# Kernel tuning notes

Measured on AMD Instinct MI355X. Metric: run time of the kernel, lower is better.

Reference implementation:

```python
import jax, jax.numpy as jnp
import numpy as np

B, T, C = 4, 2048, 2048
H, HKV = 16, 4
D = C // H            # 128
G = H // HKV          # 4 query heads per kv head
ROPE_THETA = 10000.0


def _rope_tables(seq_len, head_dim, theta):
    inv = 1.0 / (theta ** (np.arange(0, head_dim, 2, dtype=np.float32) / head_dim))
    t = np.arange(seq_len, dtype=np.float32)
    f = np.outer(t, inv)  # (T, D/2)
    return jnp.asarray(np.cos(f)), jnp.asarray(np.sin(f))


def setup_inputs() -> dict:
    key = jax.random.key(0)
    ks = jax.random.split(key, 5)
    x = jax.random.normal(ks[0], (B, T, C), dtype=jnp.float32)
    W_q = jax.random.normal(ks[1], (H * D, C), dtype=jnp.float32) * 0.02
    W_k = jax.random.normal(ks[2], (HKV * D, C), dtype=jnp.float32) * 0.02
    W_v = jax.random.normal(ks[3], (HKV * D, C), dtype=jnp.float32) * 0.02
    W_o = jax.random.normal(ks[4], (C, C), dtype=jnp.float32) * 0.02
    cos, sin = _rope_tables(T, D, ROPE_THETA)
    return {"x": x, "W_q": W_q, "W_k": W_k, "W_v": W_v, "W_o": W_o,
            "cos": cos, "sin": sin}


def _apply_rope(xh, cos, sin):
    # xh: (B, h, T, D); cos/sin: (T, D/2)
    x0 = xh[..., 0::2]
    x1 = xh[..., 1::2]
    c = cos[None, None, :, :]
    s = sin[None, None, :, :]
    o0 = x0 * c - x1 * s
    o1 = x0 * s + x1 * c
    return jnp.stack([o0, o1], axis=-1).reshape(xh.shape)


def reference(x, W_q, W_k, W_v, W_o, cos, sin):
    b, t, c = x.shape
    q = (x @ W_q.T).reshape(b, t, H, D).transpose(0, 2, 1, 3)      # (B,H,T,D)
    k = (x @ W_k.T).reshape(b, t, HKV, D).transpose(0, 2, 1, 3)    # (B,HKV,T,D)
    v = (x @ W_v.T).reshape(b, t, HKV, D).transpose(0, 2, 1, 3)
    q = _apply_rope(q, cos[:t], sin[:t])
    k = _apply_rope(k, cos[:t], sin[:t])
    # GQA via reshape instead of repeat_interleave (same head ordering:
    # q head index h = kv*G + g).
    qg = q.reshape(b, HKV, G, t, D)
    scores = jnp.einsum('bkgtd,bksd->bkgts', qg, k) / jnp.sqrt(jnp.float32(D))
    causal = jnp.tril(jnp.ones((t, t), dtype=bool))
    scores = jnp.where(causal[None, None, None, :, :], scores, -jnp.inf)
    attn = jax.nn.softmax(scores, axis=-1)
    out = jnp.einsum('bkgts,bksd->bkgtd', attn, v)                 # (B,HKV,G,T,D)
    out = out.reshape(b, H, t, D).transpose(0, 2, 1, 3).reshape(b, t, c)
    return out @ W_o.T
```

## Files before the change

kernel.cpp:

```cpp
#include <hip/hip_runtime.h>
#include <cmath>

typedef __attribute__((ext_vector_type(8))) short bf16x8;
typedef __attribute__((ext_vector_type(4))) float f32x4;
typedef __attribute__((ext_vector_type(16))) float f32x16;
typedef unsigned short u16;

__device__ __forceinline__ u16 f2bf(float f) {
  union { float f; unsigned u; } x; x.f = f;
  return (u16)((x.u + 0x7FFFu + ((x.u >> 16) & 1u)) >> 16);
}

__device__ __forceinline__ unsigned cvtpk(float lo, float hi) {
  unsigned r;
  asm("v_cvt_pk_bf16_f32 %0, %1, %2" : "=v"(r) : "v"(lo), "v"(hi));
  return r;
}

__device__ __forceinline__ void gload_lds16(const void* g, void* l) {
  __builtin_amdgcn_global_load_lds((const __attribute__((address_space(1))) unsigned*)g,
                                   (__attribute__((address_space(3))) unsigned*)l,
                                   16, 0, 0);
}

__global__ __launch_bounds__(256) void cast_all_kernel(const float* __restrict__ x,
                                                       const float* __restrict__ wq,
                                                       const float* __restrict__ wk,
                                                       const float* __restrict__ wv,
                                                       const float* __restrict__ wo,
                                                       u16* __restrict__ out) {
  const long b1 = 16777216, b2 = 20971520, b3 = 22020096, b4 = 23068672, b5 = 27262976;
  long i = (long)blockIdx.x * blockDim.x + threadIdx.x;
  long stride = (long)gridDim.x * blockDim.x;
  for (long j = i * 4; j < b5; j += stride * 4) {
    const float* src; long off;
    if (j < b1)      { src = x;  off = j; }
    else if (j < b2) { src = wq; off = j - b1; }
    else if (j < b3) { src = wk; off = j - b2; }
    else if (j < b4) { src = wv; off = j - b3; }
    else             { src = wo; off = j - b4; }
    float4 v = *(const float4*)(src + off);
    ushort4 o;
    o.x = f2bf(v.x); o.y = f2bf(v.y); o.z = f2bf(v.z); o.w = f2bf(v.w);
    *(ushort4*)(out + j) = o;
  }
}

template <int EPI>
__global__ __launch_bounds__(512, 2) void gemm_bt256(const u16* __restrict__ A,
                                                     const u16* __restrict__ B,
                                                     void* __restrict__ outp,
                                                     int M, int N, int K,
                                                     const float* __restrict__ cosp,
                                                     const float* __restrict__ sinp,
                                                     float scale) {
  __shared__ u16 lds[65536];
  const int tid = threadIdx.x;
  const int lane = tid & 63;
  const int l16 = lane & 15, lhi = lane >> 4;
  const int w = tid >> 6;
  const int wr = w >> 2, wc = w & 3;
  const int m0 = blockIdx.y * 256;
  const int n0 = blockIdx.x * 256;

  f32x4 acc[8][4];
#pragma unroll
  for (int i = 0; i < 8; ++i)
#pragma unroll
    for (int j = 0; j < 4; ++j) acc[i][j] = (f32x4)0.0f;

  const int NT = K >> 6;

  auto stage = [&](int t, int buf) {
    const int k0 = t << 6;
    u16* Ad = lds + buf * 32768;
    u16* Bd = Ad + 16384;
#pragma unroll
    for (int j = 0; j < 4; ++j) {
      int c = tid + j * 512;
      int row = c >> 3;
      int sboff = ((c & 7) * 16) ^ ((row & 7) << 4);
      gload_lds16(A + (size_t)(m0 + row) * K + k0 + (sboff >> 1), Ad + (size_t)c * 8);
    }
#pragma unroll
    for (int j = 0; j < 4; ++j) {
      int c = tid + j * 512;
      int row = c >> 3;
      int sboff = ((c & 7) * 16) ^ ((row & 7) << 4);
      gload_lds16(B + (size_t)(n0 + row) * K + k0 + (sboff >> 1), Bd + (size_t)c * 8);
    }
  };

  stage(0, 0);
  stage(1, 1);

  for (int t = 0; t < NT; ++t) {
    const int cur = t & 1;
    if (t + 1 < NT) { asm volatile("s_waitcnt vmcnt(8)" ::: "memory"); }
    else            { asm volatile("s_waitcnt vmcnt(0)" ::: "memory"); }
    __builtin_amdgcn_s_barrier();
    const char* Ab = (const char*)(lds + cur * 32768);
    const char* Bb = (const char*)(lds + cur * 32768 + 16384);
#pragma unroll
    for (int qm = 0; qm < 2; ++qm)
#pragma unroll
      for (int qn = 0; qn < 2; ++qn) {
        bf16x8 af[4][2], bfr[2][2];
#pragma unroll
        for (int mi = 0; mi < 4; ++mi) {
          int ra = wr * 128 + qm * 64 + mi * 16 + l16;
#pragma unroll
          for (int kk = 0; kk < 2; ++kk)
            af[mi][kk] = *(const bf16x8*)(Ab + ra * 128 + ((kk * 64 + lhi * 16) ^ ((ra & 7) << 4)));
        }
#pragma unroll
        for (int ni = 0; ni < 2; ++ni) {
          int rb = wc * 64 + qn * 32 + ni * 16 + l16;
#pragma unroll
          for (int kk = 0; kk < 2; ++kk)
            bfr[ni][kk] = *(const bf16x8*)(Bb + rb * 128 + ((kk * 64 + lhi * 16) ^ ((rb & 7) << 4)));
        }
        __builtin_amdgcn_s_setprio(1);
#pragma unroll
        for (int kk = 0; kk < 2; ++kk)
#pragma unroll
          for (int mi = 0; mi < 4; ++mi)
#pragma unroll
            for (int ni = 0; ni < 2; ++ni)
              acc[qm * 4 + mi][qn * 2 + ni] = __builtin_amdgcn_mfma_f32_16x16x32_bf16(
                  af[mi][kk], bfr[ni][kk], acc[qm * 4 + mi][qn * 2 + ni], 0, 0, 0);
        __builtin_amdgcn_s_setprio(0);
      }
    asm volatile("s_waitcnt lgkmcnt(0)" ::: "memory");
    __builtin_amdgcn_s_barrier();
    if (t + 2 < NT) stage(t + 2, cur);
  }

  if (EPI == 2) {
    float* o = (float*)outp;
#pragma unroll
    for (int mi8 = 0; mi8 < 8; ++mi8)
#pragma unroll
      for (int r = 0; r < 4; ++r) {
        int row = m0 + wr * 128 + mi8 * 16 + lhi * 4 + r;
#pragma unroll
        for (int nj = 0; nj < 4; ++nj) {
          int col = n0 + wc * 64 + nj * 16 + l16;
          o[(size_t)row * N + col] = acc[mi8][nj][r];
        }
      }
  } else {
    u16* o = (u16*)outp;
    const int nheads = N >> 7;
#pragma unroll
    for (int mi8 = 0; mi8 < 8; ++mi8)
#pragma unroll
      for (int r = 0; r < 4; ++r) {
        int row = m0 + wr * 128 + mi8 * 16 + lhi * 4 + r;
        int b = row >> 11;
        int tt = row & 2047;
#pragma unroll
        for (int nj = 0; nj < 4; ++nj) {
          int col = n0 + wc * 64 + nj * 16 + l16;
          int hh = col >> 7, dd = col & 127;
          float v = acc[mi8][nj][r];
          float p = __shfl_xor(v, 1);
          float c = cosp[tt * 64 + (dd >> 1)];
          float s = sinp[tt * 64 + (dd >> 1)];
          v = (lane & 1) ? fmaf(p, s, v * c) : fmaf(v, c, -p * s);
          v *= scale;
          o[((size_t)(b * nheads + hh) * 2048 + tt) * 128 + dd] = f2bf(v);
        }
      }
  }
}

template <int EPI>
__global__ __launch_bounds__(256) void gemm_bt(const u16* __restrict__ A,
                                               const u16* __restrict__ B,
                                               void* __restrict__ outp,
                                               u16* __restrict__ vtp,
                                               int M, int N, int K,
                                               const float* __restrict__ cosp,
                                               const float* __restrict__ sinp,
                                               float scale) {
  __shared__ u16 As[128 * 64];
  __shared__ u16 Bs[128 * 64];
  const int tid = threadIdx.x;
  const int lane = tid & 63;
  const int l16 = lane & 15, lhi = lane >> 4;
  const int w = tid >> 6;
  const int wr = w >> 1, wc = w & 1;
  const int m0 = blockIdx.y * 128;
  const int n0 = blockIdx.x * 128;
  const int wbase = tid - lane;

  f32x4 acc[4][4];
#pragma unroll
  for (int i = 0; i < 4; ++i)
#pragma unroll
    for (int j = 0; j < 4; ++j) acc[i][j] = (f32x4)0.0f;

  for (int k0 = 0; k0 < K; k0 += 64) {
    __syncthreads();
#pragma unroll
    for (int j = 0; j < 4; ++j) {
      int c = tid + j * 256;
      gload_lds16(A + (size_t)(m0 + (c >> 3)) * K + k0 + (c & 7) * 8,
                  As + (size_t)(wbase + j * 256) * 8);
    }
#pragma unroll
    for (int j = 0; j < 4; ++j) {
      int c = tid + j * 256;
      gload_lds16(B + (size_t)(n0 + (c >> 3)) * K + k0 + (c & 7) * 8,
                  Bs + (size_t)(wbase + j * 256) * 8);
    }
    __syncthreads();
#pragma unroll
    for (int kk = 0; kk < 64; kk += 32) {
      bf16x8 af[4], bfr[4];
#pragma unroll
      for (int mi = 0; mi < 4; ++mi)
        af[mi] = *(const bf16x8*)&As[(wr * 64 + mi * 16 + l16) * 64 + kk + lhi * 8];
#pragma unroll
      for (int ni = 0; ni < 4; ++ni)
        bfr[ni] = *(const bf16x8*)&Bs[(wc * 64 + ni * 16 + l16) * 64 + kk + lhi * 8];
#pragma unroll
      for (int mi = 0; mi < 4; ++mi)
#pragma unroll
        for (int ni = 0; ni < 4; ++ni)
          acc[mi][ni] = __builtin_amdgcn_mfma_f32_16x16x32_bf16(af[mi], bfr[ni], acc[mi][ni], 0, 0, 0);
    }
  }

  {
    const int bx = blockIdx.x;
    if (bx < 4) {
      u16* o = (u16*)outp;
#pragma unroll
      for (int mi = 0; mi < 4; ++mi)
#pragma unroll
        for (int r = 0; r < 4; ++r) {
          int row = m0 + wr * 64 + mi * 16 + lhi * 4 + r;
          int b = row >> 11;
          int t = row & 2047;
          size_t base = ((size_t)(b * 4 + bx) * 2048 + t) * 128;
#pragma unroll
          for (int ni = 0; ni < 4; ++ni) {
            int d = wc * 64 + ni * 16 + l16;
            float v = acc[mi][ni][r];
            float p = __shfl_xor(v, 1);
            float c = cosp[t * 64 + (d >> 1)];
            float s = sinp[t * 64 + (d >> 1)];
            v = (lane & 1) ? fmaf(p, s, v * c) : fmaf(v, c, -p * s);
            o[base + d] = f2bf(v);
          }
        }
    } else {
      const int kvh = bx - 4;
#pragma unroll
      for (int mi = 0; mi < 4; ++mi)
#pragma unroll
        for (int r = 0; r < 4; ++r) {
          int row = m0 + wr * 64 + mi * 16 + lhi * 4 + r;
          int b = row >> 11;
          int t = row & 2047;
          size_t base = ((size_t)(b * 4 + kvh) * 128) * 2048 + t;
#pragma unroll
          for (int ni = 0; ni < 4; ++ni) {
            int d = wc * 64 + ni * 16 + l16;
            vtp[base + (size_t)d * 2048] = f2bf(acc[mi][ni][r]);
          }
        }
    }
  }
}

__global__ __launch_bounds__(512, 2) void attn_kernel(const u16* __restrict__ Q,
                                                      const u16* __restrict__ Kp,
                                                      const u16* __restrict__ Vtp,
                                                      u16* __restrict__ O) {
  __shared__ u16 lds[65536];

  const int tid = threadIdx.x;
  const int lane = tid & 63;
  const int w = tid >> 6;
  const int l5 = lane & 31, hi = lane >> 5;
  const int bid = blockIdx.x;
  const int hb = bid & 63;
  const int pa = bid >> 6;
  const int h = hb >> 2;
  const int b = hb & 3;
  const int kvh = h >> 2;
  const int wbase = tid - lane;

  const u16* Kb = Kp + (size_t)(b * 4 + kvh) * 2048 * 128;
  const u16* Vtb = Vtp + (size_t)(b * 4 + kvh) * 128 * 2048;

  auto stageKV = [&](int kt, int buf) {
    const int t0k = kt * 128;
    u16* Kd = lds + buf * 32768;
    u16* Vd = Kd + 16384;
#pragma unroll
    for (int j = 0; j < 4; ++j) {
      int c = tid + j * 512;
      int row = c >> 4;
      int sboff = ((c & 15) * 16) ^ ((row & 15) << 4);
      gload_lds16(Kb + (size_t)(t0k + row) * 128 + (sboff >> 1),
                  Kd + (size_t)(wbase + j * 512) * 8);
    }
#pragma unroll
    for (int j = 0; j < 4; ++j) {
      int c = tid + j * 512;
      int d = c >> 4;
      int sboff = ((c & 15) * 16) ^ ((d & 7) << 4);
      gload_lds16(Vtb + (size_t)d * 2048 + t0k + (sboff >> 1),
                  Vd + (size_t)(wbase + j * 512) * 8);
    }
  };

  for (int pass = 0; pass < 2; ++pass) {
    const int qt = pass ? (7 - pa) : pa;
    const int q0 = qt * 256;
    const int wrow0 = q0 + w * 32;
    const int qg = wrow0 + l5;

    const u16* Qb = Q + ((size_t)((b * 16 + h) * 2048 + wrow0)) * 128;
    bf16x8 qf[8];
#pragma unroll
    for (int ks = 0; ks < 8; ++ks)
      qf[ks] = *(const bf16x8*)(Qb + (size_t)l5 * 128 + ks * 16 + hi * 8);

    f32x16 oacc[4];
#pragma unroll
    for (int i = 0; i < 4; ++i) oacc[i] = (f32x16)0.0f;
    float m = -3.0e38f, l = 0.0f;

    const int nkt = 2 * qt + 2;
    stageKV(0, 0);

    for (int kt = 0; kt < nkt; ++kt) {
      const int cur = kt & 1;
      if (kt + 1 < nkt) {
        stageKV(kt + 1, cur ^ 1);
        asm volatile("s_waitcnt vmcnt(8)" ::: "memory");
      } else {
        asm volatile("s_waitcnt vmcnt(0)" ::: "memory");
      }
      __builtin_amdgcn_s_barrier();

#pragma unroll
      for (int sub = 0; sub < 2; ++sub) {
        const int t0s = kt * 128 + sub * 64;
        if (t0s <= wrow0 + 31) {
          const char* ksb = (const char*)(lds + cur * 32768 + sub * 8192);
          const char* vtb = (const char*)(lds + cur * 32768 + 16384);
          const int vsub = sub * 128;

          float p[32];
#pragma unroll
          for (int kt2 = 0; kt2 < 2; ++kt2) {
            f32x16 sacc = (f32x16)0.0f;
            int row = kt2 * 32 + l5;
            __builtin_amdgcn_s_setprio(1);
#pragma unroll
            for (int ks = 0; ks < 8; ++ks) {
              bf16x8 kf = *(const bf16x8*)(ksb + row * 256 + ((ks * 32 + hi * 16) ^ ((row & 15) << 4)));
              sacc = __builtin_amdgcn_mfma_f32_32x32x16_bf16(kf, qf[ks], sacc, 0, 0, 0);
            }
            __builtin_amdgcn_s_setprio(0);
#pragma unroll
            for (int r = 0; r < 16; ++r) p[kt2 * 16 + r] = sacc[r];
          }

          if (t0s + 63 > wrow0) {
#pragma unroll
            for (int kt2 = 0; kt2 < 2; ++kt2)
#pragma unroll
              for (int r = 0; r < 16; ++r) {
                int kvg = t0s + kt2 * 32 + (r & 3) + 8 * (r >> 2) + 4 * hi;
                if (kvg > qg) p[kt2 * 16 + r] = -3.0e38f;
              }
          }

          float mx[16];
#pragma unroll
          for (int i = 0; i < 16; ++i) mx[i] = fmaxf(p[i], p[i + 16]);
#pragma unroll
          for (int i = 0; i < 8; ++i) mx[i] = fmaxf(mx[i], mx[i + 8]);
#pragma unroll
          for (int i = 0; i < 4; ++i) mx[i] = fmaxf(mx[i], mx[i + 4]);
          float rm = fmaxf(fmaxf(mx[0], mx[1]), fmaxf(mx[2], mx[3]));
          rm = fmaxf(rm, __shfl_xor(rm, 32));

          bool defer = __all(rm <= m + 8.0f);
          if (!defer) {
            float mnew = fmaxf(m, rm);
            float sc = exp2f(m - mnew);
            m = mnew;
            l *= sc;
#pragma unroll
            for (int i = 0; i < 4; ++i)
#pragma unroll
              for (int r = 0; r < 16; ++r) oacc[i][r] *= sc;
          }

#pragma unroll
          for (int i = 0; i < 32; ++i) p[i] = exp2f(p[i] - m);
          float sm[16];
#pragma unroll
          for (int i = 0; i < 16; ++i) sm[i] = p[i] + p[i + 16];
#pragma unroll
          for (int i = 0; i < 8; ++i) sm[i] += sm[i + 8];
#pragma unroll
          for (int i = 0; i < 4; ++i) sm[i] += sm[i + 4];
          float s2 = (sm[0] + sm[1]) + (sm[2] + sm[3]);
          s2 += __shfl_xor(s2, 32);
          l += s2;

#pragma unroll
          for (int kt2 = 0; kt2 < 2; ++kt2) {
#pragma unroll
            for (int sl = 0; sl < 2; ++sl) {
              int base = kt2 * 16 + sl * 8;
              unsigned A0 = cvtpk(p[base + 0], p[base + 1]);
              unsigned A1 = cvtpk(p[base + 2], p[base + 3]);
              unsigned A2 = cvtpk(p[base + 4], p[base + 5]);
              unsigned A3 = cvtpk(p[base + 6], p[base + 7]);
              asm volatile("v_permlane32_swap_b32 %0, %1" : "+v"(A0), "+v"(A2));
              asm volatile("v_permlane32_swap_b32 %0, %1" : "+v"(A1), "+v"(A3));
              union { unsigned u[4]; bf16x8 v; } pf;
              pf.u[0] = A0;
              pf.u[1] = A1;
              pf.u[2] = A2;
              pf.u[3] = A3;
              int s = kt2 * 2 + sl;
              __builtin_amdgcn_s_setprio(1);
#pragma unroll
              for (int dt = 0; dt < 4; ++dt) {
                int row = dt * 32 + l5;
                bf16x8 vb = *(const bf16x8*)(vtb + row * 256 + vsub +
                                             ((s * 32 + hi * 16) ^ ((row & 7) << 4)));
                oacc[dt] = __builtin_amdgcn_mfma_f32_32x32x16_bf16(vb, pf.v, oacc[dt], 0, 0, 0);
              }
              __builtin_amdgcn_s_setprio(0);
            }
          }
        }
      }

      asm volatile("s_waitcnt lgkmcnt(0)" ::: "memory");
      __builtin_amdgcn_s_barrier();
    }

    float inv = 1.0f / l;
    __syncthreads();
    for (int half = 0; half < 2; ++half) {
      if ((w >> 2) == half) {
        u16* OSw = lds + (w & 3) * 4352;
#pragma unroll
        for (int dt = 0; dt < 4; ++dt)
#pragma unroll
          for (int r = 0; r < 16; ++r) {
            int d = dt * 32 + (r & 3) + 8 * (r >> 2) + 4 * hi;
            OSw[l5 * 136 + d] = f2bf(oacc[dt][r] * inv);
          }
      }
      __syncthreads();
      u16* Ob = O + ((size_t)(b * 2048 + q0 + half * 128)) * 2048 + h * 128;
#pragma unroll
      for (int j = 0; j < 4; ++j) {
        int c = tid + j * 512;
        int row = c >> 4, col = c & 15;
        *(bf16x8*)(Ob + (size_t)row * 2048 + col * 8) =
            *(const bf16x8*)&lds[(row >> 5) * 4352 + (row & 31) * 136 + col * 8];
      }
      __syncthreads();
    }
  }
}

extern "C" void kernel_launch(void* const* d_in, const int* in_sizes, int n_in,
                              void* d_out, int out_size, void* d_ws, size_t ws_size,
                              hipStream_t stream) {
  (void)in_sizes; (void)n_in; (void)out_size; (void)ws_size;
  const float* x    = (const float*)d_in[0];
  const float* Wq   = (const float*)d_in[1];
  const float* Wk   = (const float*)d_in[2];
  const float* Wv   = (const float*)d_in[3];
  const float* Wo   = (const float*)d_in[4];
  const float* cosp = (const float*)d_in[5];
  const float* sinp = (const float*)d_in[6];

  u16* ws  = (u16*)d_ws;
  u16* xbf = ws;
  u16* Wqb = xbf + 16777216;
  u16* Wkb = Wqb + 4194304;
  u16* Wvb = Wkb + 1048576;
  u16* Wob = Wvb + 1048576;
  u16* Qb  = Wob + 4194304;
  u16* Kb  = Qb + 16777216;
  u16* Vb  = Kb + 4194304;
  u16* AO  = xbf;

  cast_all_kernel<<<2048, 256, 0, stream>>>(x, Wq, Wk, Wv, Wo, ws);

  const float qscale = (float)(1.4426950408889634 / sqrt(128.0));

  gemm_bt256<0><<<dim3(8, 32), 512, 0, stream>>>(xbf, Wqb, Qb, 8192, 2048, 2048, cosp, sinp, qscale);
  gemm_bt<3><<<dim3(8, 64), 256, 0, stream>>>(xbf, Wkb, Kb, Vb, 8192, 1024, 2048, cosp, sinp, 1.0f);

  attn_kernel<<<256, 512, 0, stream>>>(Qb, Kb, Vb, AO);

  gemm_bt256<2><<<dim3(8, 32), 512, 0, stream>>>(AO, Wob, d_out, 8192, 2048, 2048, nullptr, nullptr, 1.0f);
}
```

Measured before the change: 317.9 us.

## Double-buffer KV projection GEMM and widen attention softmax block to 128 keys

The K/V projection GEMM now uses two LDS buffers, issuing async global-to-LDS loads two tiles ahead with vmcnt waits in place of a full sync per step. It also raises MFMA priority and sets launch bounds for two blocks per CU. In attention, the online-softmax max, rescale and sum now run once per 128-key tile instead of once per 64-key subtile, halving the reduction and rescale overhead. The cost is more registers for the larger score array and coarser causal skipping, since a 64-key half that is fully masked is no longer skipped on its own.

```diff
diff --git a/kernel.cpp b/kernel.cpp
--- a/kernel.cpp
+++ b/kernel.cpp
@@ -175,17 +175,14 @@
   }
 }
 
-template <int EPI>
-__global__ __launch_bounds__(256) void gemm_bt(const u16* __restrict__ A,
-                                               const u16* __restrict__ B,
-                                               void* __restrict__ outp,
-                                               u16* __restrict__ vtp,
-                                               int M, int N, int K,
-                                               const float* __restrict__ cosp,
-                                               const float* __restrict__ sinp,
-                                               float scale) {
-  __shared__ u16 As[128 * 64];
-  __shared__ u16 Bs[128 * 64];
+__global__ __launch_bounds__(256, 2) void gemm_kv(const u16* __restrict__ A,
+                                                  const u16* __restrict__ B,
+                                                  u16* __restrict__ kp,
+                                                  u16* __restrict__ vtp,
+                                                  int M, int N, int K,
+                                                  const float* __restrict__ cosp,
+                                                  const float* __restrict__ sinp) {
+  __shared__ u16 lds[32768];
   const int tid = threadIdx.x;
   const int lane = tid & 63;
   const int l16 = lane & 15, lhi = lane >> 4;
@@ -201,21 +198,36 @@
 #pragma unroll
     for (int j = 0; j < 4; ++j) acc[i][j] = (f32x4)0.0f;
 
-  for (int k0 = 0; k0 < K; k0 += 64) {
-    __syncthreads();
+  const int NT = K >> 6;
+
+  auto stage = [&](int t, int buf) {
+    const int k0 = t << 6;
+    u16* Ad = lds + buf * 16384;
+    u16* Bd = Ad + 8192;
 #pragma unroll
     for (int j = 0; j < 4; ++j) {
       int c = tid + j * 256;
       gload_lds16(A + (size_t)(m0 + (c >> 3)) * K + k0 + (c & 7) * 8,
-                  As + (size_t)(wbase + j * 256) * 8);
+                  Ad + (size_t)(wbase + j * 256) * 8);
     }
 #pragma unroll
     for (int j = 0; j < 4; ++j) {
       int c = tid + j * 256;
       gload_lds16(B + (size_t)(n0 + (c >> 3)) * K + k0 + (c & 7) * 8,
-                  Bs + (size_t)(wbase + j * 256) * 8);
-    }
-    __syncthreads();
+                  Bd + (size_t)(wbase + j * 256) * 8);
+    }
+  };
+
+  stage(0, 0);
+  stage(1, 1);
+
+  for (int t = 0; t < NT; ++t) {
+    const int cur = t & 1;
+    if (t + 1 < NT) { asm volatile("s_waitcnt vmcnt(8)" ::: "memory"); }
+    else            { asm volatile("s_waitcnt vmcnt(0)" ::: "memory"); }
+    __builtin_amdgcn_s_barrier();
+    const u16* As = lds + cur * 16384;
+    const u16* Bs = As + 8192;
 #pragma unroll
     for (int kk = 0; kk < 64; kk += 32) {
       bf16x8 af[4], bfr[4];
@@ -225,18 +237,22 @@
 #pragma unroll
       for (int ni = 0; ni < 4; ++ni)
         bfr[ni] = *(const bf16x8*)&Bs[(wc * 64 + ni * 16 + l16) * 64 + kk + lhi * 8];
+      __builtin_amdgcn_s_setprio(1);
 #pragma unroll
       for (int mi = 0; mi < 4; ++mi)
 #pragma unroll
         for (int ni = 0; ni < 4; ++ni)
           acc[mi][ni] = __builtin_amdgcn_mfma_f32_16x16x32_bf16(af[mi], bfr[ni], acc[mi][ni], 0, 0, 0);
-    }
+      __builtin_amdgcn_s_setprio(0);
+    }
+    asm volatile("s_waitcnt lgkmcnt(0)" ::: "memory");
+    __builtin_amdgcn_s_barrier();
+    if (t + 2 < NT) stage(t + 2, cur);
   }
 
   {
     const int bx = blockIdx.x;
     if (bx < 4) {
-      u16* o = (u16*)outp;
 #pragma unroll
       for (int mi = 0; mi < 4; ++mi)
 #pragma unroll
@@ -253,7 +269,7 @@
             float c = cosp[t * 64 + (d >> 1)];
             float s = sinp[t * 64 + (d >> 1)];
             v = (lane & 1) ? fmaf(p, s, v * c) : fmaf(v, c, -p * s);
-            o[base + d] = f2bf(v);
+            kp[base + d] = f2bf(v);
           }
         }
     } else {
@@ -340,6 +356,7 @@
     stageKV(0, 0);
 
     for (int kt = 0; kt < nkt; ++kt) {
+      const int t0 = kt * 128;
       const int cur = kt & 1;
       if (kt + 1 < nkt) {
         stageKV(kt + 1, cur ^ 1);
@@ -349,15 +366,13 @@
       }
       __builtin_amdgcn_s_barrier();
 
-#pragma unroll
-      for (int sub = 0; sub < 2; ++sub) {
-        const int t0s = kt * 128 + sub * 64;
-        if (t0s <= wrow0 + 31) {
+      if (t0 <= wrow0 + 31) {
+        const char* vtb = (const char*)(lds + cur * 32768 + 16384);
+
+        float p[2][32];
+#pragma unroll
+        for (int sub = 0; sub < 2; ++sub) {
           const char* ksb = (const char*)(lds + cur * 32768 + sub * 8192);
-          const char* vtb = (const char*)(lds + cur * 32768 + 16384);
-          const int vsub = sub * 128;
-
-          float p[32];
 #pragma unroll
           for (int kt2 = 0; kt2 < 2; ++kt2) {
             f32x16 sacc = (f32x16)0.0f;
@@ -370,63 +385,73 @@
             }
             __builtin_amdgcn_s_setprio(0);
 #pragma unroll
-            for (int r = 0; r < 16; ++r) p[kt2 * 16 + r] = sacc[r];
+            for (int r = 0; r < 16; ++r) p[sub][kt2 * 16 + r] = sacc[r];
           }
-
-          if (t0s + 63 > wrow0) {
+        }
+
+        if (t0 + 127 > wrow0) {
+#pragma unroll
+          for (int sub = 0; sub < 2; ++sub)
 #pragma unroll
             for (int kt2 = 0; kt2 < 2; ++kt2)
 #pragma unroll
               for (int r = 0; r < 16; ++r) {
-                int kvg = t0s + kt2 * 32 + (r & 3) + 8 * (r >> 2) + 4 * hi;
-                if (kvg > qg) p[kt2 * 16 + r] = -3.0e38f;
+                int kvg = t0 + sub * 64 + kt2 * 32 + (r & 3) + 8 * (r >> 2) + 4 * hi;
+                if (kvg > qg) p[sub][kt2 * 16 + r] = -3.0e38f;
               }
-          }
-
-          float mx[16];
-#pragma unroll
-          for (int i = 0; i < 16; ++i) mx[i] = fmaxf(p[i], p[i + 16]);
-#pragma unroll
-          for (int i = 0; i < 8; ++i) mx[i] = fmaxf(mx[i], mx[i + 8]);
-#pragma unroll
-          for (int i = 0; i < 4; ++i) mx[i] = fmaxf(mx[i], mx[i + 4]);
-          float rm = fmaxf(fmaxf(mx[0], mx[1]), fmaxf(mx[2], mx[3]));
-          rm = fmaxf(rm, __shfl_xor(rm, 32));
-
-          bool defer = __all(rm <= m + 8.0f);
-          if (!defer) {
-            float mnew = fmaxf(m, rm);
-            float sc = exp2f(m - mnew);
-            m = mnew;
-            l *= sc;
-#pragma unroll
-            for (int i = 0; i < 4; ++i)
-#pragma unroll
-              for (int r = 0; r < 16; ++r) oacc[i][r] *= sc;
-          }
-
-#pragma unroll
-          for (int i = 0; i < 32; ++i) p[i] = exp2f(p[i] - m);
-          float sm[16];
-#pragma unroll
-          for (int i = 0; i < 16; ++i) sm[i] = p[i] + p[i + 16];
-#pragma unroll
-          for (int i = 0; i < 8; ++i) sm[i] += sm[i + 8];
-#pragma unroll
-          for (int i = 0; i < 4; ++i) sm[i] += sm[i + 4];
-          float s2 = (sm[0] + sm[1]) + (sm[2] + sm[3]);
-          s2 += __shfl_xor(s2, 32);
-          l += s2;
-
+        }
+
+        float mx[16];
+#pragma unroll
+        for (int i = 0; i < 16; ++i)
+          mx[i] = fmaxf(fmaxf(p[0][i], p[0][i + 16]), fmaxf(p[1][i], p[1][i + 16]));
+#pragma unroll
+        for (int i = 0; i < 8; ++i) mx[i] = fmaxf(mx[i], mx[i + 8]);
+#pragma unroll
+        for (int i = 0; i < 4; ++i) mx[i] = fmaxf(mx[i], mx[i + 4]);
+        float rm = fmaxf(fmaxf(mx[0], mx[1]), fmaxf(mx[2], mx[3]));
+        rm = fmaxf(rm, __shfl_xor(rm, 32));
+
+        bool defer = __all(rm <= m + 8.0f);
+        if (!defer) {
+          float mnew = fmaxf(m, rm);
+          float sc = exp2f(m - mnew);
+          m = mnew;
+          l *= sc;
+#pragma unroll
+          for (int i = 0; i < 4; ++i)
+#pragma unroll
+            for (int r = 0; r < 16; ++r) oacc[i][r] *= sc;
+        }
+
+#pragma unroll
+        for (int sub = 0; sub < 2; ++sub)
+#pragma unroll
+          for (int i = 0; i < 32; ++i) p[sub][i] = exp2f(p[sub][i] - m);
+        float sm[16];
+#pragma unroll
+        for (int i = 0; i < 16; ++i)
+          sm[i] = (p[0][i] + p[0][i + 16]) + (p[1][i] + p[1][i + 16]);
+#pragma unroll
+        for (int i = 0; i < 8; ++i) sm[i] += sm[i + 8];
+#pragma unroll
+        for (int i = 0; i < 4; ++i) sm[i] += sm[i + 4];
+        float s2 = (sm[0] + sm[1]) + (sm[2] + sm[3]);
+        s2 += __shfl_xor(s2, 32);
+        l += s2;
+
+#pragma unroll
+        for (int sub = 0; sub < 2; ++sub) {
+          const int vsub = sub * 128;
 #pragma unroll
           for (int kt2 = 0; kt2 < 2; ++kt2) {
 #pragma unroll
             for (int sl = 0; sl < 2; ++sl) {
               int base = kt2 * 16 + sl * 8;
-              unsigned A0 = cvtpk(p[base + 0], p[base + 1]);
-              unsigned A1 = cvtpk(p[base + 2], p[base + 3]);
-              unsigned A2 = cvtpk(p[base + 4], p[base + 5]);
-              unsigned A3 = cvtpk(p[base + 6], p[base + 7]);
+              unsigned A0 = cvtpk(p[sub][base + 0], p[sub][base + 1]);
+              unsigned A1 = cvtpk(p[sub][base + 2], p[sub][base + 3]);
+              unsigned A2 = cvtpk(p[sub][base + 4], p[sub][base + 5]);
+              unsigned A3 = cvtpk(p[sub][base + 6], p[sub][base + 7]);
               asm volatile("v_permlane32_swap_b32 %0, %1" : "+v"(A0), "+v"(A2));
               asm volatile("v_permlane32_swap_b32 %0, %1" : "+v"(A1), "+v"(A3));
               union { unsigned u[4]; bf16x8 v; } pf;
@@ -508,7 +533,7 @@
   const float qscale = (float)(1.4426950408889634 / sqrt(128.0));
 
   gemm_bt256<0><<<dim3(8, 32), 512, 0, stream>>>(xbf, Wqb, Qb, 8192, 2048, 2048, cosp, sinp, qscale);
-  gemm_bt<3><<<dim3(8, 64), 256, 0, stream>>>(xbf, Wkb, Kb, Vb, 8192, 1024, 2048, cosp, sinp, 1.0f);
+  gemm_kv<<<dim3(8, 64), 256, 0, stream>>>(xbf, Wkb, Kb, Vb, 8192, 1024, 2048, cosp, sinp);
 
   attn_kernel<<<256, 512, 0, stream>>>(Qb, Kb, Vb, AO);
 
```

New measurement: 312.8 us, median of 3. About the same (-1.6%).
